# Kernel tuning notes

Hardware: AMD Instinct MI355X
Metric: run time of the kernel (lower is better)

Reference implementation:

```python
import jax, jax.numpy as jnp
import numpy as np

NUM_EXPERTS = 4
HIDDEN = 768
INTER = 192  # expert_inter; gate_up projects to 2*INTER
TOKENS = 131072


def setup_inputs() -> dict:
    key = jax.random.key(0)
    k1, k2, k3, k4 = jax.random.split(key, 4)
    hidden = jax.random.normal(k1, (TOKENS, HIDDEN), dtype=jnp.float32)
    expert_ids = jax.random.randint(k2, (TOKENS,), 0, NUM_EXPERTS, dtype=jnp.int64)
    gate_up = jax.random.normal(k3, (NUM_EXPERTS, HIDDEN, 2 * INTER), dtype=jnp.float32) * 0.02
    down = jax.random.normal(k4, (NUM_EXPERTS, INTER, HIDDEN), dtype=jnp.float32) * 0.02
    return {"hidden": hidden, "expert_ids": expert_ids, "gate_up": gate_up, "down": down}


def reference(hidden, expert_ids, gate_up, down):
    # Math-equivalent to scatter -> per-expert SwiGLU MLP -> gather back:
    # for each token t with expert e = expert_ids[t]:
    #   out[t] = (silu(x_t @ gate_up[e][:, :F]) * (x_t @ gate_up[e][:, F:])) @ down[e]
    # With E=4 (small), compute per-expert dense and select via one-hot; this is
    # jit-friendly (static shapes) and exactly matches the per-token math.
    E = gate_up.shape[0]
    F = down.shape[1]
    onehot = (expert_ids[None, :] == jnp.arange(E)[:, None]).astype(hidden.dtype)  # [E, T]
    gu = jnp.einsum('th,ehf->etf', hidden, gate_up)      # [E, T, 2F]
    gate, up = gu[..., :F], gu[..., F:]                  # [E, T, F]
    act = jax.nn.silu(gate) * up                         # SwiGLU
    out = jnp.einsum('etf,efh,et->th', act, down, onehot)  # select token's own expert
    return out
```

## Files before the change

### kernel.cpp

```cpp
#include <hip/hip_runtime.h>
#include <hip/hip_bf16.h>

#define NE 4
#define HD 768
#define F2 384
#define F1 192
#define NT 131072
#define TT 128

typedef __attribute__((ext_vector_type(8))) short bf16x8;
typedef __attribute__((ext_vector_type(4))) float f32x4;
typedef __attribute__((ext_vector_type(4))) unsigned int u32x4;

#define SMEM_BYTES 123392
#define LTOK 122880u

#define WS_BUCKET_OFF 256
#define WS_B1IMG_OFF (WS_BUCKET_OFF + NE*NT*4)
#define WS_DNIMG_OFF (WS_B1IMG_OFF + NE*24*24576)

__device__ __forceinline__ unsigned short f2bf(float x) {
    unsigned int u = __float_as_uint(x);
    return (unsigned short)((u + 0x7fffu + ((u >> 16) & 1u)) >> 16);
}
__device__ __forceinline__ unsigned int pk2(float a, float b) {
    unsigned int ua = __float_as_uint(a), ub = __float_as_uint(b);
    unsigned int lo = (ua + 0x7fffu + ((ua >> 16) & 1u)) >> 16;
    unsigned int hi = (ub + 0x7fffu + ((ub >> 16) & 1u)) & 0xffff0000u;
    return lo | hi;
}
#define GLL(srcp, ldsoff) \
    __builtin_amdgcn_global_load_lds((const __attribute__((address_space(1))) void*)(srcp), \
        (__attribute__((address_space(3))) void*)(smem + (ldsoff)), 16, 0, 0)

__global__ void route_kernel(const int* __restrict__ ids, int* __restrict__ counts,
                             int* __restrict__ bucket) {
    __shared__ int lc[NE];
    __shared__ int lb[NE];
    int tid = threadIdx.x;
    if (tid < NE) lc[tid] = 0;
    __syncthreads();
    int t = blockIdx.x * blockDim.x + tid;
    int e = ids[t];
    int rank = atomicAdd(&lc[e], 1);
    __syncthreads();
    if (tid < NE) lb[tid] = atomicAdd(&counts[tid], lc[tid]);
    __syncthreads();
    bucket[e * NT + lb[e] + rank] = t;
}

__global__ void b1img_kernel(const float* __restrict__ gu, unsigned short* __restrict__ b1img) {
    int idx = blockIdx.x * 256 + threadIdx.x;
    int L = idx % 1536;
    int es = idx / 1536;
    int kstep = es % 24, e = es / 24;
    int colp = L >> 3, slot = L & 7;
    int v = slot ^ (colp & 7);
    int tc = colp * 2 + (v >> 2);
    int kb = kstep * 32 + (v & 3) * 8;
    const float* src = gu + ((size_t)(e * HD + kb)) * F2 + tc;
    unsigned short o[8];
    #pragma unroll
    for (int j = 0; j < 8; ++j) o[j] = f2bf(src[(size_t)j * F2]);
    *(bf16x8*)(b1img + ((size_t)idx) * 8) = *(const bf16x8*)o;
}

__global__ void dnimg_kernel(const float* __restrict__ dn, unsigned short* __restrict__ dnimg) {
    int idx = blockIdx.x * 256 + threadIdx.x;
    int L = idx % 1536;
    int r = idx / 1536;
    int kt = r % 6; r /= 6;
    int half = r & 1; int e = r >> 1;
    int colp = L >> 3, slot = L & 7;
    int v = slot ^ (colp & 7);
    int tc = colp * 2 + (v >> 2);
    int kb = kt * 32 + (v & 3) * 8;
    const float* src = dn + ((size_t)(e * F1 + kb)) * HD + half * 384 + tc;
    unsigned short o[8];
    #pragma unroll
    for (int j = 0; j < 8; ++j) o[j] = f2bf(src[(size_t)j * HD]);
    *(bf16x8*)(dnimg + ((size_t)idx) * 8) = *(const bf16x8*)o;
}

__global__ __launch_bounds__(512, 1)
void moe_kernel(const float* __restrict__ hidden, const int* __restrict__ counts,
                const int* __restrict__ bucket, const unsigned short* __restrict__ b1img,
                const unsigned short* __restrict__ dnimg, float* __restrict__ out)
{
    extern __shared__ __align__(16) unsigned char smem[];
    const unsigned LAo[2] = {0u, 8192u};
    const unsigned LBo[4] = {16384u, 40960u, 65536u, 90112u};
    const unsigned LCo[3] = {49152u, 73728u, 98304u};
    const unsigned LACT = 0u;

    int rem = blockIdx.x, e, n_e = 0;
    for (e = 0; e < NE; ++e) {
        n_e = counts[e];
        int ntiles = (n_e + TT - 1) >> 7;
        if (rem < ntiles) break;
        rem -= ntiles;
    }
    if (e >= NE) return;
    int t0 = rem << 7;

    int tid = threadIdx.x;
    int lane = tid & 63;
    int w = tid >> 6;
    int rw64 = (w >> 2) << 6;
    int cq = w & 3;
    int lg = lane >> 4;
    int l16 = lane & 15;

    int* tokp = (int*)(smem + LTOK);
    if (tid < TT) {
        int idx = t0 + tid; if (idx >= n_e) idx = n_e - 1;
        tokp[tid] = bucket[e * NT + idx];
    }
    __syncthreads();

    int arow = tid >> 2, kq = tid & 3;
    const float* aptr = hidden + (size_t)tokp[arow] * HD + kq * 8;
    unsigned awb = (unsigned)((tid >> 3) * 128 +
                   (((kq + ((arow & 1) << 2)) ^ ((tid >> 3) & 7)) << 4));

    const unsigned short* gls  = b1img + (size_t)e * 24 * 12288 + (w * 3) * 512 + lane * 8;
    const unsigned short* gls2 = dnimg + (size_t)e * 12 * 12288 + (w * 3) * 512 + lane * 8;
    unsigned gld = (unsigned)(w * 3) * 1024u;

    unsigned laneoff = (unsigned)(((l16 >> 1) << 7) +
                       (((lg + ((l16 & 1) << 2)) ^ (l16 >> 1)) << 4));
    unsigned arb[4], brb[6], b2rb[6];
    #pragma unroll
    for (int mt = 0; mt < 4; ++mt)
        arb[mt] = (unsigned)((rw64 + mt * 16) * 64) + laneoff;
    #pragma unroll
    for (int nt = 0; nt < 6; ++nt) {
        int tcb = (nt < 3) ? (cq * 48 + nt * 16) : (192 + cq * 48 + (nt - 3) * 16);
        brb[nt] = (unsigned)(tcb * 64) + laneoff;
        b2rb[nt] = (unsigned)((cq * 96 + nt * 16) * 64) + laneoff;
    }

    f32x4 avb[2][2];
    const f32x4 fzero = {0.f, 0.f, 0.f, 0.f};
    f32x4 acc[4][6];
    #pragma unroll
    for (int mt = 0; mt < 4; ++mt)
        #pragma unroll
        for (int nt = 0; nt < 6; ++nt) acc[mt][nt] = fzero;

    {
        const f32x4* p0 = (const f32x4*)(aptr);
        avb[0][0] = p0[0]; avb[0][1] = p0[1];
        const f32x4* p1 = (const f32x4*)(aptr + 32);
        avb[1][0] = p1[0]; avb[1][1] = p1[1];
        #pragma unroll
        for (int i = 0; i < 3; ++i) GLL(gls + i * 512, LBo[0] + gld + i * 1024u);
        #pragma unroll
        for (int i = 0; i < 3; ++i) GLL(gls + 12288 + i * 512, LBo[1] + gld + i * 1024u);
        u32x4 vv = {pk2(avb[0][0].x,avb[0][0].y), pk2(avb[0][0].z,avb[0][0].w),
                    pk2(avb[0][1].x,avb[0][1].y), pk2(avb[0][1].z,avb[0][1].w)};
        *(u32x4*)(smem + LAo[0] + awb) = vv;
        asm volatile("s_waitcnt vmcnt(3) lgkmcnt(0)");
        __builtin_amdgcn_s_barrier();
        __builtin_amdgcn_sched_barrier(0);
    }

    #pragma unroll
    for (int g = 0; g < 24; ++g) {
        if (g < 22) {
            const f32x4* p = (const f32x4*)(aptr + (g + 2) * 32);
            avb[g & 1][0] = p[0]; avb[g & 1][1] = p[1];
            #pragma unroll
            for (int i = 0; i < 3; ++i)
                GLL(gls + (size_t)(g + 2) * 12288 + i * 512, LBo[(g + 2) & 3] + gld + i * 1024u);
        }

        bf16x8 Af[4];
        #pragma unroll
        for (int mt = 0; mt < 4; ++mt)
            Af[mt] = *(const bf16x8*)(smem + LAo[g & 1] + arb[mt]);
        __builtin_amdgcn_s_setprio(1);
        #pragma unroll
        for (int nt = 0; nt < 6; ++nt) {
            bf16x8 Bf = *(const bf16x8*)(smem + LBo[g & 3] + brb[nt]);
            #pragma unroll
            for (int mt = 0; mt < 4; ++mt)
                acc[mt][nt] = __builtin_amdgcn_mfma_f32_16x16x32_bf16(Af[mt], Bf, acc[mt][nt], 0, 0, 0);
        }
        __builtin_amdgcn_s_setprio(0);

        if (g < 23) {
            f32x4 a0 = avb[(g + 1) & 1][0], a1 = avb[(g + 1) & 1][1];
            u32x4 vv = {pk2(a0.x,a0.y), pk2(a0.z,a0.w), pk2(a1.x,a1.y), pk2(a1.z,a1.w)};
            *(u32x4*)(smem + LAo[(g + 1) & 1] + awb) = vv;
            if (g < 22) asm volatile("s_waitcnt vmcnt(5) lgkmcnt(0)");
            else        asm volatile("s_waitcnt vmcnt(0) lgkmcnt(0)");
            __builtin_amdgcn_s_barrier();
            __builtin_amdgcn_sched_barrier(0);
        }
    }

    asm volatile("s_waitcnt lgkmcnt(0)");
    __builtin_amdgcn_s_barrier();
    __builtin_amdgcn_sched_barrier(0);

    #pragma unroll
    for (int i = 0; i < 3; ++i) GLL(gls2 + i * 512, LCo[0] + gld + i * 1024u);
    #pragma unroll
    for (int i = 0; i < 3; ++i) GLL(gls2 + 12288 + i * 512, LCo[1] + gld + i * 1024u);

    #pragma unroll
    for (int mt = 0; mt < 4; ++mt)
        #pragma unroll
        for (int nt = 0; nt < 3; ++nt)
            #pragma unroll
            for (int p = 0; p < 4; ++p) {
                float g = acc[mt][nt][p];
                float u = acc[mt][nt + 3][p];
                float s = g / (1.f + __expf(-g));
                int row = rw64 + mt * 16 + 4 * lg + p;
                int f = cq * 48 + nt * 16 + l16;
                int c = f >> 3;
                unsigned b = (unsigned)(LACT + row * 384 + (((c & 24) | ((c & 7) ^ (row & 7))) << 4) + (f & 7) * 2);
                *(unsigned short*)(smem + b) = f2bf(s * u);
            }
    asm volatile("s_waitcnt vmcnt(3) lgkmcnt(0)");
    __builtin_amdgcn_s_barrier();
    __builtin_amdgcn_sched_barrier(0);

    #pragma unroll
    for (int half = 0; half < 2; ++half) {
        f32x4 c2[4][6];
        #pragma unroll
        for (int mt = 0; mt < 4; ++mt)
            #pragma unroll
            for (int nt = 0; nt < 6; ++nt) c2[mt][nt] = fzero;

        #pragma unroll
        for (int kt = 0; kt < 6; ++kt) {
            const int s = half * 6 + kt;
            if (s < 10) {
                #pragma unroll
                for (int i = 0; i < 3; ++i)
                    GLL(gls2 + (size_t)(s + 2) * 12288 + i * 512, LCo[(s + 2) % 3] + gld + i * 1024u);
            }

            int c = kt * 4 + lg;
            unsigned a2sl = (unsigned)(((c & 24) | ((c & 7) ^ (l16 & 7))) << 4);
            bf16x8 A2[4];
            #pragma unroll
            for (int mt = 0; mt < 4; ++mt)
                A2[mt] = *(const bf16x8*)(smem + LACT + (rw64 + mt * 16 + l16) * 384 + a2sl);
            __builtin_amdgcn_s_setprio(1);
            #pragma unroll
            for (int nt = 0; nt < 6; ++nt) {
                bf16x8 B2f = *(const bf16x8*)(smem + LCo[s % 3] + b2rb[nt]);
                #pragma unroll
                for (int mt = 0; mt < 4; ++mt)
                    c2[mt][nt] = __builtin_amdgcn_mfma_f32_16x16x32_bf16(A2[mt], B2f, c2[mt][nt], 0, 0, 0);
            }
            __builtin_amdgcn_s_setprio(0);

            if (s < 11) {
                if (s < 10) asm volatile("s_waitcnt vmcnt(3) lgkmcnt(0)");
                else        asm volatile("s_waitcnt vmcnt(0) lgkmcnt(0)");
                __builtin_amdgcn_s_barrier();
                __builtin_amdgcn_sched_barrier(0);
            }
        }

        #pragma unroll
        for (int mt = 0; mt < 4; ++mt)
            #pragma unroll
            for (int p = 0; p < 4; ++p) {
                int row = rw64 + mt * 16 + 4 * lg + p;
                if (t0 + row < n_e) {
                    float* orow = out + (size_t)tokp[row] * HD + half * 384 + cq * 96 + l16;
                    #pragma unroll
                    for (int nt = 0; nt < 6; ++nt)
                        orow[nt * 16] = c2[mt][nt][p];
                }
            }
    }
}

extern "C" void kernel_launch(void* const* d_in, const int* in_sizes, int n_in,
                              void* d_out, int out_size, void* d_ws, size_t ws_size,
                              hipStream_t stream) {
    (void)in_sizes; (void)n_in; (void)out_size; (void)ws_size;
    const float* hidden = (const float*)d_in[0];
    const int*   ids    = (const int*)d_in[1];
    const float* gu     = (const float*)d_in[2];
    const float* dn     = (const float*)d_in[3];
    float* out = (float*)d_out;

    char* ws = (char*)d_ws;
    int* counts = (int*)ws;
    int* bucket = (int*)(ws + WS_BUCKET_OFF);
    unsigned short* b1img = (unsigned short*)(ws + WS_B1IMG_OFF);
    unsigned short* dnimg = (unsigned short*)(ws + WS_DNIMG_OFF);

    hipMemsetAsync(d_ws, 0, 64, stream);
    route_kernel<<<NT / 256, 256, 0, stream>>>(ids, counts, bucket);
    b1img_kernel<<<576, 256, 0, stream>>>(gu, b1img);
    dnimg_kernel<<<288, 256, 0, stream>>>(dn, dnimg);
    moe_kernel<<<1028, 512, SMEM_BYTES, stream>>>(hidden, counts, bucket, b1img, dnimg, out);
}
```

Baseline: 287.2 us.

## Halve token tile to 64 and run two blocks per CU with smaller LDS

Shrinks the per-block token tile from 128 to 64, halves per-wave accumulators, and cuts LDS so two 512-thread blocks can share a CU (launch bounds 512,2, grid doubled). The B-operand pipelines drop from 4/3-stage to 2-stage double buffering with full vmcnt(0) waits each step. The SwiGLU activation moves to a separate pass that reads bf16 gate/up values back from LDS, since each wave now owns only gate or only up columns. The aim is better latency hiding through occupancy. The cost is that each weight tile is now loaded for half as many tokens, doubling weight traffic, plus shallower prefetch and an extra bf16 rounding of gate/up before the activation.

New measurement: 303.7 us. 1.06x slower.

```diff
diff --git a/kernel.cpp b/kernel.cpp
--- a/kernel.cpp
+++ b/kernel.cpp
@@ -6,14 +6,23 @@
 #define F2 384
 #define F1 192
 #define NT 131072
-#define TT 128
+#define TT 64
 
 typedef __attribute__((ext_vector_type(8))) short bf16x8;
 typedef __attribute__((ext_vector_type(4))) float f32x4;
 typedef __attribute__((ext_vector_type(4))) unsigned int u32x4;
-
-#define SMEM_BYTES 123392
-#define LTOK 122880u
+typedef __attribute__((ext_vector_type(2))) unsigned int u32x2;
+
+#define LAB0 0u
+#define LAB1 4608u
+#define LB10 9216u
+#define LB11 33792u
+#define LGU  24576u
+#define LACT 0u
+#define LC0  24576u
+#define LC1  49152u
+#define LTOK 73728u
+#define SMEM_BYTES 73984
 
 #define WS_BUCKET_OFF 256
 #define WS_B1IMG_OFF (WS_BUCKET_OFF + NE*NT*4)
@@ -28,6 +37,9 @@
     unsigned int lo = (ua + 0x7fffu + ((ua >> 16) & 1u)) >> 16;
     unsigned int hi = (ub + 0x7fffu + ((ub >> 16) & 1u)) & 0xffff0000u;
     return lo | hi;
+}
+__device__ __forceinline__ float bf2f(unsigned short s) {
+    return __uint_as_float(((unsigned int)s) << 16);
 }
 #define GLL(srcp, ldsoff) \
     __builtin_amdgcn_global_load_lds((const __attribute__((address_space(1))) void*)(srcp), \
@@ -82,32 +94,26 @@
     *(bf16x8*)(dnimg + ((size_t)idx) * 8) = *(const bf16x8*)o;
 }
 
-__global__ __launch_bounds__(512, 1)
+__global__ __launch_bounds__(512, 2)
 void moe_kernel(const float* __restrict__ hidden, const int* __restrict__ counts,
                 const int* __restrict__ bucket, const unsigned short* __restrict__ b1img,
                 const unsigned short* __restrict__ dnimg, float* __restrict__ out)
 {
     extern __shared__ __align__(16) unsigned char smem[];
-    const unsigned LAo[2] = {0u, 8192u};
-    const unsigned LBo[4] = {16384u, 40960u, 65536u, 90112u};
-    const unsigned LCo[3] = {49152u, 73728u, 98304u};
-    const unsigned LACT = 0u;
 
     int rem = blockIdx.x, e, n_e = 0;
     for (e = 0; e < NE; ++e) {
         n_e = counts[e];
-        int ntiles = (n_e + TT - 1) >> 7;
+        int ntiles = (n_e + TT - 1) >> 6;
         if (rem < ntiles) break;
         rem -= ntiles;
     }
     if (e >= NE) return;
-    int t0 = rem << 7;
+    int t0 = rem << 6;
 
     int tid = threadIdx.x;
     int lane = tid & 63;
     int w = tid >> 6;
-    int rw64 = (w >> 2) << 6;
-    int cq = w & 3;
     int lg = lane >> 4;
     int l16 = lane & 15;
 
@@ -118,143 +124,158 @@
     }
     __syncthreads();
 
-    int arow = tid >> 2, kq = tid & 3;
-    const float* aptr = hidden + (size_t)tokp[arow] * HD + kq * 8;
-    unsigned awb = (unsigned)((tid >> 3) * 128 +
-                   (((kq + ((arow & 1) << 2)) ^ ((tid >> 3) & 7)) << 4));
+    int ar = tid >> 3, kq = tid & 7;
+    const float* aptr = hidden + (size_t)tokp[ar] * HD + kq * 4;
+    unsigned awb = (unsigned)(ar * 72 + (((kq >> 1) ^ (ar & 3)) << 4) + (kq & 1) * 8);
 
     const unsigned short* gls  = b1img + (size_t)e * 24 * 12288 + (w * 3) * 512 + lane * 8;
     const unsigned short* gls2 = dnimg + (size_t)e * 12 * 12288 + (w * 3) * 512 + lane * 8;
     unsigned gld = (unsigned)(w * 3) * 1024u;
 
+    unsigned arb[4];
+    #pragma unroll
+    for (int mt = 0; mt < 4; ++mt)
+        arb[mt] = (unsigned)((mt * 16 + l16) * 72 + ((lg ^ (l16 & 3)) << 4));
     unsigned laneoff = (unsigned)(((l16 >> 1) << 7) +
                        (((lg + ((l16 & 1) << 2)) ^ (l16 >> 1)) << 4));
-    unsigned arb[4], brb[6], b2rb[6];
+    unsigned brb[3];
+    #pragma unroll
+    for (int nt = 0; nt < 3; ++nt)
+        brb[nt] = (unsigned)((w * 48 + nt * 16) * 64) + laneoff;
+
+    f32x4 av;
+    auto issueA = [&](int g) { av = *(const f32x4*)(aptr + g * 32); };
+    auto writeA = [&](unsigned base) {
+        u32x2 vv = {pk2(av.x, av.y), pk2(av.z, av.w)};
+        *(u32x2*)(smem + base + awb) = vv;
+    };
+
+    const f32x4 fzero = {0.f, 0.f, 0.f, 0.f};
+    f32x4 acc[4][3];
     #pragma unroll
     for (int mt = 0; mt < 4; ++mt)
-        arb[mt] = (unsigned)((rw64 + mt * 16) * 64) + laneoff;
-    #pragma unroll
-    for (int nt = 0; nt < 6; ++nt) {
-        int tcb = (nt < 3) ? (cq * 48 + nt * 16) : (192 + cq * 48 + (nt - 3) * 16);
-        brb[nt] = (unsigned)(tcb * 64) + laneoff;
-        b2rb[nt] = (unsigned)((cq * 96 + nt * 16) * 64) + laneoff;
-    }
-
-    f32x4 avb[2][2];
-    const f32x4 fzero = {0.f, 0.f, 0.f, 0.f};
-    f32x4 acc[4][6];
-    #pragma unroll
-    for (int mt = 0; mt < 4; ++mt)
-        #pragma unroll
-        for (int nt = 0; nt < 6; ++nt) acc[mt][nt] = fzero;
-
-    {
-        const f32x4* p0 = (const f32x4*)(aptr);
-        avb[0][0] = p0[0]; avb[0][1] = p0[1];
-        const f32x4* p1 = (const f32x4*)(aptr + 32);
-        avb[1][0] = p1[0]; avb[1][1] = p1[1];
-        #pragma unroll
-        for (int i = 0; i < 3; ++i) GLL(gls + i * 512, LBo[0] + gld + i * 1024u);
-        #pragma unroll
-        for (int i = 0; i < 3; ++i) GLL(gls + 12288 + i * 512, LBo[1] + gld + i * 1024u);
-        u32x4 vv = {pk2(avb[0][0].x,avb[0][0].y), pk2(avb[0][0].z,avb[0][0].w),
-                    pk2(avb[0][1].x,avb[0][1].y), pk2(avb[0][1].z,avb[0][1].w)};
-        *(u32x4*)(smem + LAo[0] + awb) = vv;
-        asm volatile("s_waitcnt vmcnt(3) lgkmcnt(0)");
-        __builtin_amdgcn_s_barrier();
-        __builtin_amdgcn_sched_barrier(0);
-    }
-
-    #pragma unroll
+        #pragma unroll
+        for (int nt = 0; nt < 3; ++nt) acc[mt][nt] = fzero;
+
+    issueA(0);
+    #pragma unroll
+    for (int i = 0; i < 3; ++i) GLL(gls + i * 512, LB10 + gld + i * 1024u);
+    writeA(LAB0);
+    asm volatile("s_waitcnt vmcnt(0) lgkmcnt(0)");
+    __builtin_amdgcn_s_barrier();
+    __builtin_amdgcn_sched_barrier(0);
+
+    #pragma unroll 1
     for (int g = 0; g < 24; ++g) {
-        if (g < 22) {
-            const f32x4* p = (const f32x4*)(aptr + (g + 2) * 32);
-            avb[g & 1][0] = p[0]; avb[g & 1][1] = p[1];
+        unsigned Ab  = (g & 1) ? LAB1 : LAB0;
+        unsigned Bb  = (g & 1) ? LB11 : LB10;
+        unsigned Abn = (g & 1) ? LAB0 : LAB1;
+        unsigned Bbn = (g & 1) ? LB10 : LB11;
+        if (g < 23) {
+            issueA(g + 1);
             #pragma unroll
             for (int i = 0; i < 3; ++i)
-                GLL(gls + (size_t)(g + 2) * 12288 + i * 512, LBo[(g + 2) & 3] + gld + i * 1024u);
+                GLL(gls + (size_t)(g + 1) * 12288 + i * 512, Bbn + gld + i * 1024u);
         }
 
         bf16x8 Af[4];
         #pragma unroll
         for (int mt = 0; mt < 4; ++mt)
-            Af[mt] = *(const bf16x8*)(smem + LAo[g & 1] + arb[mt]);
+            Af[mt] = *(const bf16x8*)(smem + Ab + arb[mt]);
         __builtin_amdgcn_s_setprio(1);
         #pragma unroll
-        for (int nt = 0; nt < 6; ++nt) {
-            bf16x8 Bf = *(const bf16x8*)(smem + LBo[g & 3] + brb[nt]);
+        for (int nt = 0; nt < 3; ++nt) {
+            bf16x8 Bf = *(const bf16x8*)(smem + Bb + brb[nt]);
             #pragma unroll
             for (int mt = 0; mt < 4; ++mt)
                 acc[mt][nt] = __builtin_amdgcn_mfma_f32_16x16x32_bf16(Af[mt], Bf, acc[mt][nt], 0, 0, 0);
         }
         __builtin_amdgcn_s_setprio(0);
 
-        if (g < 23) {
-            f32x4 a0 = avb[(g + 1) & 1][0], a1 = avb[(g + 1) & 1][1];
-            u32x4 vv = {pk2(a0.x,a0.y), pk2(a0.z,a0.w), pk2(a1.x,a1.y), pk2(a1.z,a1.w)};
-            *(u32x4*)(smem + LAo[(g + 1) & 1] + awb) = vv;
-            if (g < 22) asm volatile("s_waitcnt vmcnt(5) lgkmcnt(0)");
-            else        asm volatile("s_waitcnt vmcnt(0) lgkmcnt(0)");
-            __builtin_amdgcn_s_barrier();
-            __builtin_amdgcn_sched_barrier(0);
+        if (g < 23) writeA(Abn);
+        asm volatile("s_waitcnt vmcnt(0) lgkmcnt(0)");
+        __builtin_amdgcn_s_barrier();
+        __builtin_amdgcn_sched_barrier(0);
+    }
+
+    #pragma unroll
+    for (int mt = 0; mt < 4; ++mt)
+        #pragma unroll
+        for (int nt = 0; nt < 3; ++nt)
+            #pragma unroll
+            for (int p = 0; p < 4; ++p) {
+                int row = mt * 16 + 4 * lg + p;
+                int vc = w * 48 + nt * 16 + l16;
+                int c = vc >> 3;
+                unsigned b = (unsigned)(LGU + row * 768 +
+                             (((c & ~7) | ((c & 7) ^ (row & 7))) << 4) + (vc & 7) * 2);
+                *(unsigned short*)(smem + b) = f2bf(acc[mt][nt][p]);
+            }
+    asm volatile("s_waitcnt lgkmcnt(0)");
+    __builtin_amdgcn_s_barrier();
+
+    {
+        int r = tid >> 3, q = tid & 7;
+        #pragma unroll
+        for (int j3 = 0; j3 < 3; ++j3) {
+            int c = q * 3 + j3;
+            unsigned gb = (unsigned)(LGU + r * 768 + (((c & ~7) | ((c & 7) ^ (r & 7))) << 4));
+            bf16x8 gv = *(const bf16x8*)(smem + gb);
+            bf16x8 uv = *(const bf16x8*)(smem + gb + 384u);
+            unsigned int o[4];
+            #pragma unroll
+            for (int j = 0; j < 4; ++j) {
+                float g0 = bf2f((unsigned short)gv[2 * j]);
+                float g1 = bf2f((unsigned short)gv[2 * j + 1]);
+                float u0 = bf2f((unsigned short)uv[2 * j]);
+                float u1 = bf2f((unsigned short)uv[2 * j + 1]);
+                float a0 = g0 / (1.f + __expf(-g0)) * u0;
+                float a1 = g1 / (1.f + __expf(-g1)) * u1;
+                o[j] = pk2(a0, a1);
+            }
+            unsigned ab = (unsigned)(LACT + r * 384 + (((c & ~7) | ((c & 7) ^ (r & 7))) << 4));
+            *(u32x4*)(smem + ab) = *(u32x4*)o;
         }
     }
-
     asm volatile("s_waitcnt lgkmcnt(0)");
     __builtin_amdgcn_s_barrier();
     __builtin_amdgcn_sched_barrier(0);
 
     #pragma unroll
-    for (int i = 0; i < 3; ++i) GLL(gls2 + i * 512, LCo[0] + gld + i * 1024u);
-    #pragma unroll
-    for (int i = 0; i < 3; ++i) GLL(gls2 + 12288 + i * 512, LCo[1] + gld + i * 1024u);
-
-    #pragma unroll
-    for (int mt = 0; mt < 4; ++mt)
-        #pragma unroll
-        for (int nt = 0; nt < 3; ++nt)
-            #pragma unroll
-            for (int p = 0; p < 4; ++p) {
-                float g = acc[mt][nt][p];
-                float u = acc[mt][nt + 3][p];
-                float s = g / (1.f + __expf(-g));
-                int row = rw64 + mt * 16 + 4 * lg + p;
-                int f = cq * 48 + nt * 16 + l16;
-                int c = f >> 3;
-                unsigned b = (unsigned)(LACT + row * 384 + (((c & 24) | ((c & 7) ^ (row & 7))) << 4) + (f & 7) * 2);
-                *(unsigned short*)(smem + b) = f2bf(s * u);
-            }
-    asm volatile("s_waitcnt vmcnt(3) lgkmcnt(0)");
+    for (int i = 0; i < 3; ++i) GLL(gls2 + i * 512, LC0 + gld + i * 1024u);
+    asm volatile("s_waitcnt vmcnt(0)");
     __builtin_amdgcn_s_barrier();
     __builtin_amdgcn_sched_barrier(0);
 
     #pragma unroll
     for (int half = 0; half < 2; ++half) {
-        f32x4 c2[4][6];
+        f32x4 c2[4][3];
         #pragma unroll
         for (int mt = 0; mt < 4; ++mt)
             #pragma unroll
-            for (int nt = 0; nt < 6; ++nt) c2[mt][nt] = fzero;
+            for (int nt = 0; nt < 3; ++nt) c2[mt][nt] = fzero;
 
         #pragma unroll
         for (int kt = 0; kt < 6; ++kt) {
             const int s = half * 6 + kt;
-            if (s < 10) {
+            unsigned Cb = (s & 1) ? LC1 : LC0;
+            if (s < 11) {
+                unsigned Cbn = (s & 1) ? LC0 : LC1;
                 #pragma unroll
                 for (int i = 0; i < 3; ++i)
-                    GLL(gls2 + (size_t)(s + 2) * 12288 + i * 512, LCo[(s + 2) % 3] + gld + i * 1024u);
+                    GLL(gls2 + (size_t)(s + 1) * 12288 + i * 512, Cbn + gld + i * 1024u);
             }
 
             int c = kt * 4 + lg;
-            unsigned a2sl = (unsigned)(((c & 24) | ((c & 7) ^ (l16 & 7))) << 4);
+            unsigned a2sl = (unsigned)((((c & 24) | ((c & 7) ^ (l16 & 7)))) << 4);
             bf16x8 A2[4];
             #pragma unroll
             for (int mt = 0; mt < 4; ++mt)
-                A2[mt] = *(const bf16x8*)(smem + LACT + (rw64 + mt * 16 + l16) * 384 + a2sl);
+                A2[mt] = *(const bf16x8*)(smem + LACT + (mt * 16 + l16) * 384 + a2sl);
             __builtin_amdgcn_s_setprio(1);
             #pragma unroll
-            for (int nt = 0; nt < 6; ++nt) {
-                bf16x8 B2f = *(const bf16x8*)(smem + LCo[s % 3] + b2rb[nt]);
+            for (int nt = 0; nt < 3; ++nt) {
+                bf16x8 B2f = *(const bf16x8*)(smem + Cb + brb[nt] - (unsigned)0);
                 #pragma unroll
                 for (int mt = 0; mt < 4; ++mt)
                     c2[mt][nt] = __builtin_amdgcn_mfma_f32_16x16x32_bf16(A2[mt], B2f, c2[mt][nt], 0, 0, 0);
@@ -262,8 +283,7 @@
             __builtin_amdgcn_s_setprio(0);
 
             if (s < 11) {
-                if (s < 10) asm volatile("s_waitcnt vmcnt(3) lgkmcnt(0)");
-                else        asm volatile("s_waitcnt vmcnt(0) lgkmcnt(0)");
+                asm volatile("s_waitcnt vmcnt(0) lgkmcnt(0)");
                 __builtin_amdgcn_s_barrier();
                 __builtin_amdgcn_sched_barrier(0);
             }
@@ -273,11 +293,11 @@
         for (int mt = 0; mt < 4; ++mt)
             #pragma unroll
             for (int p = 0; p < 4; ++p) {
-                int row = rw64 + mt * 16 + 4 * lg + p;
+                int row = mt * 16 + 4 * lg + p;
                 if (t0 + row < n_e) {
-                    float* orow = out + (size_t)tokp[row] * HD + half * 384 + cq * 96 + l16;
+                    float* orow = out + (size_t)tokp[row] * HD + half * 384 + w * 48 + l16;
                     #pragma unroll
-                    for (int nt = 0; nt < 6; ++nt)
+                    for (int nt = 0; nt < 3; ++nt)
                         orow[nt * 16] = c2[mt][nt][p];
                 }
             }
@@ -304,5 +324,5 @@
     route_kernel<<<NT / 256, 256, 0, stream>>>(ids, counts, bucket);
     b1img_kernel<<<576, 256, 0, stream>>>(gu, b1img);
     dnimg_kernel<<<288, 256, 0, stream>>>(dn, dnimg);
-    moe_kernel<<<1028, 512, SMEM_BYTES, stream>>>(hidden, counts, bucket, b1img, dnimg, out);
-}
+    moe_kernel<<<2052, 512, SMEM_BYTES, stream>>>(hidden, counts, bucket, b1img, dnimg, out);
+}
```
